# Optimization experiments

Hardware: AMD Instinct MI355X
Metric: run time of the kernel (lower is better)

The kernel has to match this reference:

```python
import jax, jax.numpy as jnp
import numpy as np

VOCAB = 32000
EMBED = 512
HIDDEN = 512
SEQ = 4096


def setup_inputs() -> dict:
    key = jax.random.key(0)
    ks = jax.random.split(key, 20)
    s = 1.0 / np.sqrt(HIDDEN)

    def n(k, shape):
        return (jax.random.normal(k, shape, dtype=jnp.float32) * s).astype(jnp.float32)

    inp = {}
    inp["input"] = jax.random.randint(ks[0], (SEQ,), 0, VOCAB)
    inp["embed_w"] = n(ks[1], (VOCAB, EMBED))
    # layer 0 (input size EMBED), forward and backward directions; gate order i,f,g,o
    inp["Wih0f"] = n(ks[2], (4 * HIDDEN, EMBED))
    inp["Whh0f"] = n(ks[3], (4 * HIDDEN, HIDDEN))
    inp["b0f"] = n(ks[4], (4 * HIDDEN,))  # b_ih + b_hh combined (same math)
    inp["Wih0b"] = n(ks[5], (4 * HIDDEN, EMBED))
    inp["Whh0b"] = n(ks[6], (4 * HIDDEN, HIDDEN))
    inp["b0b"] = n(ks[7], (4 * HIDDEN,))
    # layer 1 (input size 2*HIDDEN)
    inp["Wih1f"] = n(ks[8], (4 * HIDDEN, 2 * HIDDEN))
    inp["Whh1f"] = n(ks[9], (4 * HIDDEN, HIDDEN))
    inp["b1f"] = n(ks[10], (4 * HIDDEN,))
    inp["Wih1b"] = n(ks[11], (4 * HIDDEN, 2 * HIDDEN))
    inp["Whh1b"] = n(ks[12], (4 * HIDDEN, HIDDEN))
    inp["b1b"] = n(ks[13], (4 * HIDDEN,))
    # output head
    inp["Wlin"] = n(ks[14], (VOCAB, 2 * HIDDEN))
    inp["blin"] = n(ks[15], (VOCAB,))
    return inp


def _lstm_dir(xproj, Whh, reverse):
    # xproj: [S, 4H] = x @ Wih.T + b, precomputed outside the scan.
    H = Whh.shape[1]
    WhhT = Whh.T  # [H, 4H]

    def step(carry, xp):
        h, c = carry
        g = xp + h @ WhhT  # [4H]
        i, f, gg, o = jnp.split(g, 4)
        i = jax.nn.sigmoid(i)
        f = jax.nn.sigmoid(f)
        gg = jnp.tanh(gg)
        o = jax.nn.sigmoid(o)
        c = f * c + i * gg
        h = o * jnp.tanh(c)
        return (h, c), h

    h0 = jnp.zeros((H,), xproj.dtype)
    _, hs = jax.lax.scan(step, (h0, h0), xproj, reverse=reverse)
    return hs  # [S, H], aligned to original time order


def _bilstm_layer(x, Wihf, Whhf, bf, Wihb, Whhb, bb):
    hf = _lstm_dir(x @ Wihf.T + bf, Whhf, reverse=False)
    hb = _lstm_dir(x @ Wihb.T + bb, Whhb, reverse=True)
    return jnp.concatenate([hf, hb], axis=-1)  # [S, 2H]


def reference(input, embed_w, Wih0f, Whh0f, b0f, Wih0b, Whh0b, b0b,
              Wih1f, Whh1f, b1f, Wih1b, Whh1b, b1b, Wlin, blin):
    x = embed_w[input]  # [S, E]  (batch=1 squeezed away; same math)
    x = _bilstm_layer(x, Wih0f, Whh0f, b0f, Wih0b, Whh0b, b0b)
    x = _bilstm_layer(x, Wih1f, Whh1f, b1f, Wih1b, Whh1b, b1b)
    out = x @ Wlin.T + blin  # [S, VOCAB]
    return out
```

## Files before the change

kernel.cpp:

```cpp
#include <hip/hip_runtime.h>
#include <hip/hip_bf16.h>
#include <stdint.h>

#define S_LEN 4096

typedef __attribute__((ext_vector_type(8))) short short8;
typedef __attribute__((ext_vector_type(4))) float f32x4;

__device__ inline unsigned short f2bf(float f) {
  unsigned int x = __float_as_uint(f);
  x += 0x7fffu + ((x >> 16) & 1u);
  return (unsigned short)(x >> 16);
}

__device__ inline float sigm(float x) { return 1.0f / (1.0f + __expf(-x)); }
__device__ inline float tanhf_(float x) {
  float e = __expf(-2.0f * fabsf(x));
  float t = (1.0f - e) / (1.0f + e);
  return copysignf(t, x);
}

__device__ inline void gload_lds16(const void* g, void* l) {
  __builtin_amdgcn_global_load_lds(
      (const __attribute__((address_space(1))) unsigned int*)g,
      (__attribute__((address_space(3))) unsigned int*)l, 16, 0, 0);
}

__global__ void embed_kernel(const int* __restrict__ idx, const float* __restrict__ E,
                             unsigned short* __restrict__ x0b) {
  const int row = blockIdx.x;
  const int t = threadIdx.x;
  const int id = idx[row];
  f32x4 v = ((const f32x4*)(E + (size_t)id * 512))[t];
  ushort4 u;
  u.x = f2bf(v[0]); u.y = f2bf(v[1]); u.z = f2bf(v[2]); u.w = f2bf(v[3]);
  ((ushort4*)(x0b + (size_t)row * 512))[t] = u;
}

__global__ void f32_to_bf16_kernel(const float* __restrict__ src, unsigned short* __restrict__ dst) {
  const size_t i = (size_t)blockIdx.x * blockDim.x + threadIdx.x;
  f32x4 v = ((const f32x4*)src)[i];
  ushort4 u;
  u.x = f2bf(v[0]); u.y = f2bf(v[1]); u.z = f2bf(v[2]); u.w = f2bf(v[3]);
  ((ushort4*)dst)[i] = u;
}

template <bool BF32>
__global__ __launch_bounds__(256) void gemm_bt(
    const unsigned short* __restrict__ A,
    const void* __restrict__ Bsrc,
    const float* __restrict__ bias,
    float* __restrict__ C,
    int M, int N, int K)
{
  __shared__ unsigned short Al[128 * 32];
  __shared__ unsigned short Bl[128 * 32];
  const int tiles_n = N >> 7;
  const int tm = (blockIdx.x / tiles_n) << 7;
  const int tn = (blockIdx.x % tiles_n) << 7;
  const int t = threadIdx.x;
  const int w = t >> 6, l = t & 63;
  const int wr = w >> 1, wc = w & 1;

  f32x4 acc[4][4] = {};

  for (int k0 = 0; k0 < K; k0 += 32) {
    __syncthreads();
    {
      const int rb = w * 32;
      const unsigned short* ga = A + (size_t)(tm + rb + (l >> 2)) * K + k0 + (l & 3) * 8;
      gload_lds16(ga, &Al[rb * 32]);
      gload_lds16(ga + (size_t)16 * K, &Al[(rb + 16) * 32]);
    }
    if constexpr (!BF32) {
      const unsigned short* B = (const unsigned short*)Bsrc;
      const int rb = w * 32;
      const unsigned short* gb = B + (size_t)(tn + rb + (l >> 2)) * K + k0 + (l & 3) * 8;
      gload_lds16(gb, &Bl[rb * 32]);
      gload_lds16(gb + (size_t)16 * K, &Bl[(rb + 16) * 32]);
    } else {
      const float* B = (const float*)Bsrc;
      const int row = t >> 1, half = t & 1;
      const f32x4* src = (const f32x4*)(B + (size_t)(tn + row) * K + k0 + half * 16);
      f32x4 v0 = src[0], v1 = src[1], v2 = src[2], v3 = src[3];
      short8 p0, p1;
      p0[0] = f2bf(v0[0]); p0[1] = f2bf(v0[1]); p0[2] = f2bf(v0[2]); p0[3] = f2bf(v0[3]);
      p0[4] = f2bf(v1[0]); p0[5] = f2bf(v1[1]); p0[6] = f2bf(v1[2]); p0[7] = f2bf(v1[3]);
      p1[0] = f2bf(v2[0]); p1[1] = f2bf(v2[1]); p1[2] = f2bf(v2[2]); p1[3] = f2bf(v2[3]);
      p1[4] = f2bf(v3[0]); p1[5] = f2bf(v3[1]); p1[6] = f2bf(v3[2]); p1[7] = f2bf(v3[3]);
      *(short8*)&Bl[row * 32 + half * 16] = p0;
      *(short8*)&Bl[row * 32 + half * 16 + 8] = p1;
    }
    __syncthreads();

    const int lrow = l & 15;
    const int lkb = (l >> 4) * 8;
    short8 af[4], bfr[4];
    #pragma unroll
    for (int fm = 0; fm < 4; fm++)
      af[fm] = *(const short8*)&Al[(wr * 64 + fm * 16 + lrow) * 32 + lkb];
    #pragma unroll
    for (int fn = 0; fn < 4; fn++)
      bfr[fn] = *(const short8*)&Bl[(wc * 64 + fn * 16 + lrow) * 32 + lkb];
    #pragma unroll
    for (int fm = 0; fm < 4; fm++)
      #pragma unroll
      for (int fn = 0; fn < 4; fn++)
        acc[fm][fn] = __builtin_amdgcn_mfma_f32_16x16x32_bf16(af[fm], bfr[fn], acc[fm][fn], 0, 0, 0);
  }

  const int r0 = tm + wr * 64;
  const int c0 = tn + wc * 64 + (l & 15);
  const int rbase = (l >> 4) * 4;
  #pragma unroll
  for (int fm = 0; fm < 4; fm++) {
    #pragma unroll
    for (int fn = 0; fn < 4; fn++) {
      const int col = c0 + fn * 16;
      const float bv = bias ? bias[col] : 0.0f;
      #pragma unroll
      for (int rg = 0; rg < 4; rg++) {
        const int rr = r0 + fm * 16 + rbase + rg;
        C[(size_t)rr * N + col] = acc[fm][fn][rg] + bv;
      }
    }
  }
}

__global__ __launch_bounds__(512, 2) void lstm_layer(
    const float* __restrict__ WhhF, const float* __restrict__ WhhB,
    const float* __restrict__ biasF, const float* __restrict__ biasB,
    const float* __restrict__ xproj,
    unsigned int* __restrict__ Hx,
    unsigned short* __restrict__ Hb)
{
  const int S = S_LEN;
  const int dir = blockIdx.x & 1;
  const int chunk = blockIdx.x >> 1;
  const float* Whh = dir ? WhhB : WhhF;
  const float* bias = dir ? biasB : biasF;
  const int t = threadIdx.x;
  const int w = t >> 6, l = t & 63;
  const int g = l >> 4;
  const int jl = (l >> 3) & 1;
  const int o = l & 7;
  const int elem = w * 2 + jl;
  const int r = g * 512 + chunk * 16 + elem;
  const int xoff = dir * 2048, hoff = dir * 512;

  f32x4 w4[16];
  {
    const f32x4* wp = (const f32x4*)(Whh + (size_t)r * 512 + o * 64);
    #pragma unroll
    for (int i = 0; i < 16; i++) w4[i] = wp[i];
  }
  const float bv = bias[r];

  __shared__ float hsh[2][8 * 68];
  float c = 0.0f;
  const int slot = (t >> 6) * 68 + (t & 63);

  float xp_cur = 0.0f;
  if (o == 0) {
    const int t0 = dir ? (S - 1) : 0;
    xp_cur = xproj[(size_t)t0 * 4096 + xoff + r] + bv;
  }

  for (int st = 0; st < S; st++) {
    const int tcur = dir ? (S - 1 - st) : st;
    const int pp = st & 1;

    float xp_nxt = 0.0f;
    if (o == 0 && st + 1 < S) {
      const int tn = dir ? (S - 2 - st) : (st + 1);
      xp_nxt = xproj[(size_t)tn * 4096 + xoff + r] + bv;
    }

    if (st == 0) {
      hsh[0][slot] = 0.0f;
    } else {
      const int tprev = dir ? (tcur + 1) : (tcur - 1);
      const unsigned int* src = Hx + (size_t)tprev * 1024 + hoff + t;
      unsigned int v;
      int cap = 1 << 16;
      do {
        v = __hip_atomic_load(src, __ATOMIC_RELAXED, __HIP_MEMORY_SCOPE_AGENT);
      } while (v == 0xFFFFFFFFu && --cap > 0);
      hsh[pp][slot] = __uint_as_float(v);
    }
    __syncthreads();

    float acc = 0.0f;
    const f32x4* hp = (const f32x4*)&hsh[pp][o * 68];
    #pragma unroll
    for (int i = 0; i < 16; i++) {
      f32x4 h4 = hp[i];
      f32x4 ww = w4[i];
      acc = fmaf(ww[0], h4[0], acc);
      acc = fmaf(ww[1], h4[1], acc);
      acc = fmaf(ww[2], h4[2], acc);
      acc = fmaf(ww[3], h4[3], acc);
    }
    acc += __shfl_xor(acc, 1);
    acc += __shfl_xor(acc, 2);
    acc += __shfl_xor(acc, 4);
    acc += xp_cur;

    const float av = (g == 2) ? tanhf_(acc) : sigm(acc);
    const float f_ = __shfl(av, (l & 8) + 16);
    const float g_ = __shfl(av, (l & 8) + 32);
    const float o_ = __shfl(av, (l & 8) + 48);

    if ((l & 55) == 0) {
      c = f_ * c + av * g_;
      const float h = o_ * tanhf_(c);
      const size_t ofs = (size_t)tcur * 1024 + hoff + chunk * 16 + elem;
      __hip_atomic_store(Hx + ofs, __float_as_uint(h),
                         __ATOMIC_RELAXED, __HIP_MEMORY_SCOPE_AGENT);
      Hb[ofs] = f2bf(h);
    }
    xp_cur = xp_nxt;
  }
}

extern "C" void kernel_launch(void* const* d_in, const int* in_sizes, int n_in,
                              void* d_out, int out_size, void* d_ws, size_t ws_size,
                              hipStream_t stream) {
  (void)in_sizes; (void)n_in; (void)out_size; (void)ws_size;
  const int*   input   = (const int*)d_in[0];
  const float* embed_w = (const float*)d_in[1];
  const float* Wih0f   = (const float*)d_in[2];
  const float* Whh0f   = (const float*)d_in[3];
  const float* b0f     = (const float*)d_in[4];
  const float* Wih0b   = (const float*)d_in[5];
  const float* Whh0b   = (const float*)d_in[6];
  const float* b0b     = (const float*)d_in[7];
  const float* Wih1f   = (const float*)d_in[8];
  const float* Whh1f   = (const float*)d_in[9];
  const float* b1f     = (const float*)d_in[10];
  const float* Wih1b   = (const float*)d_in[11];
  const float* Whh1b   = (const float*)d_in[12];
  const float* b1b     = (const float*)d_in[13];
  const float* Wlin    = (const float*)d_in[14];
  const float* blin    = (const float*)d_in[15];

  char* ws = (char*)d_ws;
  unsigned short* x0b   = (unsigned short*)(ws);
  unsigned short* Wih0  = (unsigned short*)(ws + ((size_t)4  << 20));
  unsigned short* Wih1  = (unsigned short*)(ws + ((size_t)8  << 20));
  unsigned short* H0b   = (unsigned short*)(ws + ((size_t)16 << 20));
  unsigned short* H1b   = (unsigned short*)(ws + ((size_t)24 << 20));

  float* dout  = (float*)d_out;
  float* xproj = dout;
  unsigned int* H0 = (unsigned int*)(dout + ((size_t)16 << 20));
  unsigned int* H1 = (unsigned int*)(dout + ((size_t)20 << 20));

  hipMemsetAsync(H0, 0xFF, (size_t)8 * 1024 * 1024 * 4, stream);

  embed_kernel<<<4096, 128, 0, stream>>>(input, embed_w, x0b);

  f32_to_bf16_kernel<<<1024, 256, 0, stream>>>(Wih0f, Wih0);
  f32_to_bf16_kernel<<<1024, 256, 0, stream>>>(Wih0b, Wih0 + (size_t)2048 * 512);
  f32_to_bf16_kernel<<<2048, 256, 0, stream>>>(Wih1f, Wih1);
  f32_to_bf16_kernel<<<2048, 256, 0, stream>>>(Wih1b, Wih1 + (size_t)2048 * 1024);

  gemm_bt<false><<<32 * 32, 256, 0, stream>>>(x0b, Wih0, nullptr, xproj, 4096, 4096, 512);
  lstm_layer<<<64, 512, 0, stream>>>(Whh0f, Whh0b, b0f, b0b, xproj, H0, H0b);

  gemm_bt<false><<<32 * 32, 256, 0, stream>>>(H0b, Wih1, nullptr, xproj, 4096, 4096, 1024);
  lstm_layer<<<64, 512, 0, stream>>>(Whh1f, Whh1b, b1f, b1b, xproj, H1, H1b);

  gemm_bt<true><<<32 * 250, 256, 0, stream>>>(H1b, Wlin, blin, dout, 4096, 32000, 1024);
}
```

Baseline: 12.07 ms.

## Split LSTM recurrence across 128 smaller blocks with 64-bit h exchange

The persistent LSTM kernel now launches 128 blocks of 256 threads instead of 64 blocks of 512. Each block owns 8 hidden elements instead of 16, and the whole wave computes the cell update. Hidden-state exchange uses 64-bit atomic loads and stores of element pairs, which halves the number of polled words, and the prior-h load is issued before the per-step work. Recurrent weights are no longer held in registers but reloaded from global or L2 every step. That cuts register pressure but adds per-step memory traffic, and the grid-wide spin synchronisation now spans more blocks.

```diff
diff --git a/kernel.cpp b/kernel.cpp
--- a/kernel.cpp
+++ b/kernel.cpp
@@ -6,6 +6,7 @@
 
 typedef __attribute__((ext_vector_type(8))) short short8;
 typedef __attribute__((ext_vector_type(4))) float f32x4;
+typedef __attribute__((ext_vector_type(2))) float f32x2;
 
 __device__ inline unsigned short f2bf(float f) {
   unsigned int x = __float_as_uint(f);
@@ -127,7 +128,7 @@
   }
 }
 
-__global__ __launch_bounds__(512, 2) void lstm_layer(
+__global__ __launch_bounds__(256, 1) void lstm_layer(
     const float* __restrict__ WhhF, const float* __restrict__ WhhB,
     const float* __restrict__ biasF, const float* __restrict__ biasB,
     const float* __restrict__ xproj,
@@ -141,24 +142,18 @@
   const float* bias = dir ? biasB : biasF;
   const int t = threadIdx.x;
   const int w = t >> 6, l = t & 63;
-  const int g = l >> 4;
-  const int jl = (l >> 3) & 1;
   const int o = l & 7;
-  const int elem = w * 2 + jl;
-  const int r = g * 512 + chunk * 16 + elem;
+  const int g = (l >> 3) & 3;
+  const int e = t >> 5;
+  const int r = g * 512 + chunk * 8 + e;
   const int xoff = dir * 2048, hoff = dir * 512;
 
-  f32x4 w4[16];
-  {
-    const f32x4* wp = (const f32x4*)(Whh + (size_t)r * 512 + o * 64);
-    #pragma unroll
-    for (int i = 0; i < 16; i++) w4[i] = wp[i];
-  }
+  const f32x4* wp = (const f32x4*)(Whh + (size_t)r * 512 + o * 64);
   const float bv = bias[r];
 
   __shared__ float hsh[2][8 * 68];
   float c = 0.0f;
-  const int slot = (t >> 6) * 68 + (t & 63);
+  const int slot2 = (t >> 5) * 68 + ((2 * t) & 63);
 
   float xp_cur = 0.0f;
   if (o == 0) {
@@ -169,6 +164,17 @@
   for (int st = 0; st < S; st++) {
     const int tcur = dir ? (S - 1 - st) : st;
     const int pp = st & 1;
+    const int tprev = dir ? (tcur + 1) : (tcur - 1);
+
+    const unsigned long long* src =
+        (const unsigned long long*)(Hx + (size_t)tprev * 1024 + hoff) + t;
+    unsigned long long v = 0;
+    if (st > 0)
+      v = __hip_atomic_load(src, __ATOMIC_RELAXED, __HIP_MEMORY_SCOPE_AGENT);
+
+    f32x4 wv[16];
+    #pragma unroll
+    for (int j = 0; j < 16; j++) wv[j] = wp[j];
 
     float xp_nxt = 0.0f;
     if (o == 0 && st + 1 < S) {
@@ -177,25 +183,23 @@
     }
 
     if (st == 0) {
-      hsh[0][slot] = 0.0f;
+      *(f32x2*)&hsh[0][slot2] = f32x2{0.0f, 0.0f};
     } else {
-      const int tprev = dir ? (tcur + 1) : (tcur - 1);
-      const unsigned int* src = Hx + (size_t)tprev * 1024 + hoff + t;
-      unsigned int v;
       int cap = 1 << 16;
-      do {
+      while (((v >> 32) == 0xFFFFFFFFull || (v & 0xFFFFFFFFull) == 0xFFFFFFFFull)
+             && --cap > 0)
         v = __hip_atomic_load(src, __ATOMIC_RELAXED, __HIP_MEMORY_SCOPE_AGENT);
-      } while (v == 0xFFFFFFFFu && --cap > 0);
-      hsh[pp][slot] = __uint_as_float(v);
+      *(f32x2*)&hsh[pp][slot2] =
+          f32x2{__uint_as_float((unsigned int)v), __uint_as_float((unsigned int)(v >> 32))};
     }
     __syncthreads();
 
     float acc = 0.0f;
-    const f32x4* hp = (const f32x4*)&hsh[pp][o * 68];
+    const float* hb = &hsh[pp][o * 68];
     #pragma unroll
     for (int i = 0; i < 16; i++) {
-      f32x4 h4 = hp[i];
-      f32x4 ww = w4[i];
+      f32x4 h4 = *(const f32x4*)&hb[4 * i];
+      f32x4 ww = wv[i];
       acc = fmaf(ww[0], h4[0], acc);
       acc = fmaf(ww[1], h4[1], acc);
       acc = fmaf(ww[2], h4[2], acc);
@@ -207,17 +211,24 @@
     acc += xp_cur;
 
     const float av = (g == 2) ? tanhf_(acc) : sigm(acc);
-    const float f_ = __shfl(av, (l & 8) + 16);
-    const float g_ = __shfl(av, (l & 8) + 32);
-    const float o_ = __shfl(av, (l & 8) + 48);
-
-    if ((l & 55) == 0) {
-      c = f_ * c + av * g_;
-      const float h = o_ * tanhf_(c);
-      const size_t ofs = (size_t)tcur * 1024 + hoff + chunk * 16 + elem;
-      __hip_atomic_store(Hx + ofs, __float_as_uint(h),
+    const int l0 = l & 32;
+    const float f_ = __shfl(av, l0 + 8);
+    const float g_ = __shfl(av, l0 + 16);
+    const float o_ = __shfl(av, l0 + 24);
+
+    c = f_ * c + av * g_;
+    const float h = o_ * tanhf_(c);
+    const float hpair = __shfl(h, l | 32);
+
+    if (l == 0) {
+      const size_t eofs = (size_t)tcur * 1024 + hoff + chunk * 8 + 2 * w;
+      const unsigned long long pk =
+          (unsigned long long)__float_as_uint(h) |
+          ((unsigned long long)__float_as_uint(hpair) << 32);
+      __hip_atomic_store((unsigned long long*)(Hx + eofs), pk,
                          __ATOMIC_RELAXED, __HIP_MEMORY_SCOPE_AGENT);
-      Hb[ofs] = f2bf(h);
+      const unsigned int hb2 = (unsigned int)f2bf(h) | ((unsigned int)f2bf(hpair) << 16);
+      *(unsigned int*)(Hb + eofs) = hb2;
     }
     xp_cur = xp_nxt;
   }
@@ -266,10 +277,10 @@
   f32_to_bf16_kernel<<<2048, 256, 0, stream>>>(Wih1b, Wih1 + (size_t)2048 * 1024);
 
   gemm_bt<false><<<32 * 32, 256, 0, stream>>>(x0b, Wih0, nullptr, xproj, 4096, 4096, 512);
-  lstm_layer<<<64, 512, 0, stream>>>(Whh0f, Whh0b, b0f, b0b, xproj, H0, H0b);
+  lstm_layer<<<128, 256, 0, stream>>>(Whh0f, Whh0b, b0f, b0b, xproj, H0, H0b);
 
   gemm_bt<false><<<32 * 32, 256, 0, stream>>>(H0b, Wih1, nullptr, xproj, 4096, 4096, 1024);
-  lstm_layer<<<64, 512, 0, stream>>>(Whh1f, Whh1b, b1f, b1b, xproj, H1, H1b);
+  lstm_layer<<<128, 256, 0, stream>>>(Whh1f, Whh1b, b1f, b1b, xproj, H1, H1b);
 
   gemm_bt<true><<<32 * 250, 256, 0, stream>>>(H1b, Wlin, blin, dout, 4096, 32000, 1024);
 }
```

Measured after the change: 21.25 ms. 1.76x slower.
